# Optimization experiments

Measured on AMD Instinct MI355X. Metric: run time of the kernel, lower is better.

## Reference

```python
import jax, jax.numpy as jnp
import numpy as np

B, N, D, K, NUM_ITERS, EPS = 256, 4096, 64, 16, 3, 1e-8
LN_EPS = 1e-5


def ln(x, g, b):
    m = jnp.mean(x, axis=-1, keepdims=True)
    v = jnp.mean(jnp.square(x - m), axis=-1, keepdims=True)
    return (x - m) * jax.lax.rsqrt(v + LN_EPS) * g + b


def setup_inputs() -> dict:
    key = jax.random.key(0)
    ks = jax.random.split(key, 12)
    w = lambda k, s: jax.random.normal(k, s, dtype=jnp.float32) * 0.02
    return {
        "inputs": jax.random.normal(ks[0], (B, N, D), dtype=jnp.float32),
        "mask": jnp.ones((B, N), dtype=bool),
        "noise": jax.random.normal(ks[1], (B, K, D), dtype=jnp.float32),
        "slot_mu": w(ks[2], (1, 1, D)),
        "slot_logvar": jnp.zeros((1, 1, D), dtype=jnp.float32),
        "wq": w(ks[3], (D, D)), "bq": jnp.zeros((D,), jnp.float32),
        "wk": w(ks[4], (D, D)), "bk": jnp.zeros((D,), jnp.float32),
        "wv": w(ks[5], (D, D)), "bv": jnp.zeros((D,), jnp.float32),
        "w_ih": w(ks[6], (3 * D, D)), "w_hh": w(ks[7], (3 * D, D)),
        "b_ih": jnp.zeros((3 * D,), jnp.float32), "b_hh": jnp.zeros((3 * D,), jnp.float32),
        "g_in": jnp.ones((D,), jnp.float32), "b_in": jnp.zeros((D,), jnp.float32),
        "g_sl": jnp.ones((D,), jnp.float32), "b_sl": jnp.zeros((D,), jnp.float32),
        "g_mlp": jnp.ones((D,), jnp.float32), "b_mlp": jnp.zeros((D,), jnp.float32),
        "w1": w(ks[8], (2 * D, D)), "b1": jnp.zeros((2 * D,), jnp.float32),
        "w2": w(ks[9], (D, 2 * D)), "b2": jnp.zeros((D,), jnp.float32),
    }


def reference(inputs, mask, noise, slot_mu, slot_logvar, wq, bq, wk, bk, wv, bv,
              w_ih, w_hh, b_ih, b_hh, g_in, b_in, g_sl, b_sl, g_mlp, b_mlp,
              w1, b1, w2, b2):
    scale = D ** (-0.5)
    # init slots from learned Gaussian (noise passed explicitly for determinism)
    slots = slot_mu + jnp.exp(0.5 * slot_logvar) * noise  # (B,K,D)
    x = ln(inputs, g_in, b_in)
    k = x @ wk.T + bk  # (B,N,D)
    v = x @ wv.T + bv
    neg = jnp.where(mask, 0.0, -1e9).astype(x.dtype)[:, None, :]  # (B,1,N)

    def attend(s):
        q = ln(s, g_sl, b_sl) @ wq.T + bq
        logits = jnp.einsum('bkd,bnd->bkn', q, k) * scale + neg
        return jax.nn.softmax(logits, axis=1)  # competition over slots

    for _ in range(NUM_ITERS):
        slots_prev = slots
        attn = attend(slots)
        attn = attn + EPS
        attn = attn / jnp.sum(attn, axis=-1, keepdims=True)
        upd = jnp.einsum('bkn,bnd->bkd', attn, v)
        # torch GRUCell: gates order r, z, n
        gx = upd @ w_ih.T + b_ih          # (B,K,3D)
        gh = slots_prev @ w_hh.T + b_hh
        xr, xz, xn = jnp.split(gx, 3, axis=-1)
        hr, hz, hn = jnp.split(gh, 3, axis=-1)
        r = jax.nn.sigmoid(xr + hr)
        z = jax.nn.sigmoid(xz + hz)
        n = jnp.tanh(xn + r * hn)
        slots = (1.0 - z) * n + z * slots_prev
        h = ln(slots, g_mlp, b_mlp)
        slots = slots + jax.nn.relu(h @ w1.T + b1) @ w2.T + b2

    attn = attend(slots)
    return slots, attn
```

## Files before the change

kernel.cpp:

```cpp
#include <hip/hip_runtime.h>
#include <hip/hip_bf16.h>
#include <stdint.h>

#define B_ 256
#define N_ 4096
#define D_ 64
#define K_ 16
#define EPS_ 1e-8f
#define LN_EPS_ 1e-5f

typedef __attribute__((ext_vector_type(8))) short short8;
typedef __attribute__((ext_vector_type(4))) float f32x4;

__device__ __forceinline__ unsigned short f2bf(float f) {
  unsigned u = __builtin_bit_cast(unsigned, f);
  u += 0x7fffu + ((u >> 16) & 1u);
  return (unsigned short)(u >> 16);
}

__device__ __forceinline__ float sum4(f32x4 x) { return x[0] + x[1] + x[2] + x[3]; }

__device__ __forceinline__ float wsum64(float v) {
  v += __shfl_xor(v, 1); v += __shfl_xor(v, 2); v += __shfl_xor(v, 4);
  v += __shfl_xor(v, 8); v += __shfl_xor(v, 16); v += __shfl_xor(v, 32);
  return v;
}

template<int MODE, int LOADBF, int STORECACHE>
__global__ __launch_bounds__(256)
void attend2(const float* __restrict__ inputs,
             unsigned short* __restrict__ xcache,
             const float* __restrict__ g_in, const float* __restrict__ b_in,
             const float* __restrict__ q2w, const float* __restrict__ qcw,
             float* __restrict__ U, float* __restrict__ S,
             float* __restrict__ attn_out)
{
  const int b = blockIdx.y;
  const int chunk = blockIdx.x;
  const int wave = threadIdx.x >> 6;
  const int lane = threadIdx.x & 63;
  const int n = lane & 15;
  const int quad = lane >> 4;

  __shared__ unsigned short xbt[4][64][40];
  __shared__ unsigned short pbuf[4][16][40];
  __shared__ float redS[4][16];

  const float* qp = q2w + b * 1024 + n * 64 + quad * 8;
  short8 qa0, qa1;
#pragma unroll
  for (int j = 0; j < 8; ++j) {
    qa0[j] = (short)f2bf(qp[j]);
    qa1[j] = (short)f2bf(qp[32 + j]);
  }
  float qc[4];
#pragma unroll
  for (int r = 0; r < 4; ++r) qc[r] = qcw[b * 16 + quad * 4 + r];

  f32x4 gi[4], bi[4];
  if constexpr (!LOADBF) {
    gi[0] = *(const f32x4*)(g_in + quad * 8);       gi[1] = *(const f32x4*)(g_in + quad * 8 + 4);
    gi[2] = *(const f32x4*)(g_in + 32 + quad * 8);  gi[3] = *(const f32x4*)(g_in + 36 + quad * 8);
    bi[0] = *(const f32x4*)(b_in + quad * 8);       bi[1] = *(const f32x4*)(b_in + quad * 8 + 4);
    bi[2] = *(const f32x4*)(b_in + 32 + quad * 8);  bi[3] = *(const f32x4*)(b_in + 36 + quad * 8);
  }

  f32x4 Uacc[4];
#pragma unroll
  for (int t = 0; t < 4; ++t) Uacc[t] = (f32x4){0.f, 0.f, 0.f, 0.f};
  float Sacc[4] = {0.f, 0.f, 0.f, 0.f};

  const int rowwave = chunk * 1024 + wave * 256;

  for (int g = 0; g < 8; ++g) {
#pragma unroll
    for (int sub = 0; sub < 2; ++sub) {
      const int row = rowwave + g * 32 + sub * 16 + n;
      short8 xlo, xhi;
      if constexpr (LOADBF) {
        const unsigned short* xp = xcache + ((size_t)(b * N_ + row)) * 64 + quad * 8;
        xlo = __builtin_bit_cast(short8, *(const f32x4*)xp);
        xhi = __builtin_bit_cast(short8, *(const f32x4*)(xp + 32));
      } else {
        const float* bp = inputs + ((size_t)(b * N_ + row)) * 64;
        f32x4 a0 = *(const f32x4*)(bp + quad * 8);
        f32x4 a1 = *(const f32x4*)(bp + quad * 8 + 4);
        f32x4 a2 = *(const f32x4*)(bp + 32 + quad * 8);
        f32x4 a3 = *(const f32x4*)(bp + 36 + quad * 8);
        float s = sum4(a0) + sum4(a1) + sum4(a2) + sum4(a3);
        s += __shfl_xor(s, 16); s += __shfl_xor(s, 32);
        const float m = s * (1.f / 64.f);
        f32x4 d0 = a0 - m, d1 = a1 - m, d2 = a2 - m, d3 = a3 - m;
        float v = sum4(d0 * d0) + sum4(d1 * d1) + sum4(d2 * d2) + sum4(d3 * d3);
        v += __shfl_xor(v, 16); v += __shfl_xor(v, 32);
        const float rs = rsqrtf(v * (1.f / 64.f) + LN_EPS_);
        f32x4 y0 = d0 * rs * gi[0] + bi[0];
        f32x4 y1 = d1 * rs * gi[1] + bi[1];
        f32x4 y2 = d2 * rs * gi[2] + bi[2];
        f32x4 y3 = d3 * rs * gi[3] + bi[3];
#pragma unroll
        for (int j = 0; j < 4; ++j) {
          xlo[j]     = (short)f2bf(y0[j]);
          xlo[4 + j] = (short)f2bf(y1[j]);
          xhi[j]     = (short)f2bf(y2[j]);
          xhi[4 + j] = (short)f2bf(y3[j]);
        }
        if constexpr (STORECACHE) {
          unsigned short* sp = xcache + ((size_t)(b * N_ + row)) * 64 + quad * 8;
          *(f32x4*)sp = __builtin_bit_cast(f32x4, xlo);
          *(f32x4*)(sp + 32) = __builtin_bit_cast(f32x4, xhi);
        }
      }

      f32x4 c = __builtin_amdgcn_mfma_f32_16x16x32_bf16(qa0, xlo, (f32x4){0.f, 0.f, 0.f, 0.f}, 0, 0, 0);
      c = __builtin_amdgcn_mfma_f32_16x16x32_bf16(qa1, xhi, c, 0, 0, 0);

      float l[4];
#pragma unroll
      for (int r = 0; r < 4; ++r) l[r] = (c[r] + qc[r]) * 0.125f;
      float mx = fmaxf(fmaxf(l[0], l[1]), fmaxf(l[2], l[3]));
      mx = fmaxf(mx, __shfl_xor(mx, 16));
      mx = fmaxf(mx, __shfl_xor(mx, 32));
      float e[4], es = 0.f;
#pragma unroll
      for (int r = 0; r < 4; ++r) { e[r] = __expf(l[r] - mx); es += e[r]; }
      es += __shfl_xor(es, 16); es += __shfl_xor(es, 32);
      const float rinv = 1.f / es;

      if constexpr (MODE == 2) {
#pragma unroll
        for (int r = 0; r < 4; ++r)
          attn_out[((size_t)b * 16 + quad * 4 + r) * N_ + row] = e[r] * rinv;
      } else {
#pragma unroll
        for (int r = 0; r < 4; ++r) {
          const float p = e[r] * rinv;
          Sacc[r] += p;
          pbuf[wave][quad * 4 + r][sub * 16 + n] = f2bf(p);
        }
#pragma unroll
        for (int j = 0; j < 8; ++j) {
          xbt[wave][quad * 8 + j][sub * 16 + n]      = (unsigned short)xlo[j];
          xbt[wave][32 + quad * 8 + j][sub * 16 + n] = (unsigned short)xhi[j];
        }
      }
    }

    if constexpr (MODE != 2) {
      short8 pa = *(const short8*)&pbuf[wave][n][quad * 8];
#pragma unroll
      for (int t = 0; t < 4; ++t) {
        short8 bx = *(const short8*)&xbt[wave][t * 16 + n][quad * 8];
        Uacc[t] = __builtin_amdgcn_mfma_f32_16x16x32_bf16(pa, bx, Uacc[t], 0, 0, 0);
      }
    }
  }

  if constexpr (MODE == 2) return;

#pragma unroll
  for (int r = 0; r < 4; ++r) {
    float sv = Sacc[r];
    sv += __shfl_xor(sv, 1); sv += __shfl_xor(sv, 2);
    sv += __shfl_xor(sv, 4); sv += __shfl_xor(sv, 8);
    if (n == 0) redS[wave][quad * 4 + r] = sv;
  }
  __syncthreads();
  float* red = (float*)&xbt[0][0][0];
#pragma unroll
  for (int t = 0; t < 4; ++t)
#pragma unroll
    for (int r = 0; r < 4; ++r)
      red[(t * 4 + r) * 256 + wave * 64 + lane] = Uacc[t][r];
  __syncthreads();
#pragma unroll
  for (int ii = 0; ii < 4; ++ii) {
    const int i = wave * 4 + ii;
    const float sum = red[i * 256 + lane] + red[i * 256 + 64 + lane] +
                      red[i * 256 + 128 + lane] + red[i * 256 + 192 + lane];
    const int t = i >> 2, r = i & 3;
    atomicAdd(&U[b * 1024 + (quad * 4 + r) * 64 + t * 16 + n], sum);
  }
  if (threadIdx.x < 16) {
    const float ss = redS[0][threadIdx.x] + redS[1][threadIdx.x] +
                     redS[2][threadIdx.x] + redS[3][threadIdx.x];
    atomicAdd(&S[b * 16 + threadIdx.x], ss);
  }
}

__global__ __launch_bounds__(256)
void mid_kernel(int iter,
                const float* __restrict__ noise, const float* __restrict__ mu,
                const float* __restrict__ logvar,
                const float* __restrict__ wq, const float* __restrict__ bq,
                const float* __restrict__ wk, const float* __restrict__ bk,
                const float* __restrict__ wv, const float* __restrict__ bv,
                const float* __restrict__ w_ih, const float* __restrict__ w_hh,
                const float* __restrict__ b_ih, const float* __restrict__ b_hh,
                const float* __restrict__ g_sl, const float* __restrict__ b_sl,
                const float* __restrict__ g_mlp, const float* __restrict__ b_mlp,
                const float* __restrict__ w1, const float* __restrict__ b1,
                const float* __restrict__ w2, const float* __restrict__ b2,
                float* __restrict__ slots_ws, float* __restrict__ q2w, float* __restrict__ qcw,
                const float* __restrict__ U, const float* __restrict__ S,
                float* __restrict__ out_slots)
{
  const int b = blockIdx.x;
  const int tid = threadIdx.x;
  __shared__ float sl[1024];
  __shared__ float snew[1024];
  __shared__ float updx[1024];
  __shared__ float upds[1024];
  __shared__ float gx[3072];
  __shared__ float gh[3072];
  __shared__ float hh[1024];
  __shared__ float t1[2048];
  __shared__ float qv[1024];

  if (iter == 0) {
    for (int idx = tid; idx < 1024; idx += 256) {
      int d = idx & 63;
      snew[idx] = mu[d] + expf(0.5f * logvar[d]) * noise[(size_t)b * 1024 + idx];
    }
    __syncthreads();
  } else {
    for (int idx = tid; idx < 1024; idx += 256) sl[idx] = slots_ws[b * 1024 + idx];
    for (int idx = tid; idx < 1024; idx += 256) {
      int kk = idx >> 6;
      float denom = S[b * 16 + kk] + (float)N_ * EPS_;
      updx[idx] = U[b * 1024 + idx] / denom;
    }
    __syncthreads();
    for (int idx = tid; idx < 1024; idx += 256) {
      int kk = idx >> 6, d = idx & 63;
      float acc = bv[d];
      for (int e = 0; e < 64; ++e) acc += updx[kk * 64 + e] * wv[d * 64 + e];
      upds[idx] = acc;
    }
    __syncthreads();
    for (int idx = tid; idx < 3072; idx += 256) {
      int kk = idx / 192, j = idx % 192;
      float ax = b_ih[j], ah = b_hh[j];
      for (int d = 0; d < 64; ++d) {
        ax += upds[kk * 64 + d] * w_ih[j * 64 + d];
        ah += sl[kk * 64 + d] * w_hh[j * 64 + d];
      }
      gx[idx] = ax;
      gh[idx] = ah;
    }
    __syncthreads();
    for (int idx = tid; idx < 1024; idx += 256) {
      int kk = idx >> 6, d = idx & 63;
      float xr_ = gx[kk * 192 + d], xz_ = gx[kk * 192 + 64 + d], xn_ = gx[kk * 192 + 128 + d];
      float hr_ = gh[kk * 192 + d], hz_ = gh[kk * 192 + 64 + d], hn_ = gh[kk * 192 + 128 + d];
      float r_ = 1.f / (1.f + expf(-(xr_ + hr_)));
      float z_ = 1.f / (1.f + expf(-(xz_ + hz_)));
      float n_ = tanhf(xn_ + r_ * hn_);
      snew[idx] = (1.f - z_) * n_ + z_ * sl[idx];
    }
    __syncthreads();
    {
      int wv_ = tid >> 6, lane = tid & 63;
      for (int kk = wv_; kk < 16; kk += 4) {
        float v = snew[kk * 64 + lane];
        float m = wsum64(v) * (1.f / 64.f);
        float dd = v - m;
        float var = wsum64(dd * dd) * (1.f / 64.f);
        hh[kk * 64 + lane] = dd * rsqrtf(var + LN_EPS_) * g_mlp[lane] + b_mlp[lane];
      }
    }
    __syncthreads();
    for (int idx = tid; idx < 2048; idx += 256) {
      int kk = idx >> 7, j = idx & 127;
      float acc = b1[j];
      for (int d = 0; d < 64; ++d) acc += hh[kk * 64 + d] * w1[j * 64 + d];
      t1[idx] = fmaxf(acc, 0.f);
    }
    __syncthreads();
    for (int idx = tid; idx < 1024; idx += 256) {
      int kk = idx >> 6, d = idx & 63;
      float acc = b2[d];
      for (int j = 0; j < 128; ++j) acc += t1[kk * 128 + j] * w2[d * 128 + j];
      snew[idx] += acc;
    }
    __syncthreads();
  }

  for (int idx = tid; idx < 1024; idx += 256) {
    slots_ws[b * 1024 + idx] = snew[idx];
    if (iter == 3) out_slots[b * 1024 + idx] = snew[idx];
  }
  {
    int wv_ = tid >> 6, lane = tid & 63;
    for (int kk = wv_; kk < 16; kk += 4) {
      float v = snew[kk * 64 + lane];
      float m = wsum64(v) * (1.f / 64.f);
      float dd = v - m;
      float var = wsum64(dd * dd) * (1.f / 64.f);
      hh[kk * 64 + lane] = dd * rsqrtf(var + LN_EPS_) * g_sl[lane] + b_sl[lane];
    }
  }
  __syncthreads();
  for (int idx = tid; idx < 1024; idx += 256) {
    int kk = idx >> 6, d = idx & 63;
    float acc = bq[d];
    for (int e = 0; e < 64; ++e) acc += hh[kk * 64 + e] * wq[d * 64 + e];
    qv[idx] = acc;
  }
  __syncthreads();
  for (int idx = tid; idx < 1024; idx += 256) {
    int kk = idx >> 6, e = idx & 63;
    float acc = 0.f;
    for (int d = 0; d < 64; ++d) acc += qv[kk * 64 + d] * wk[d * 64 + e];
    q2w[b * 1024 + idx] = acc;
  }
  if (tid < 16) {
    float acc = 0.f;
    for (int d = 0; d < 64; ++d) acc += qv[tid * 64 + d] * bk[d];
    qcw[b * 16 + tid] = acc;
  }
}

extern "C" void kernel_launch(void* const* d_in, const int* in_sizes, int n_in,
                              void* d_out, int out_size, void* d_ws, size_t ws_size,
                              hipStream_t stream) {
  const float* inputs = (const float*)d_in[0];
  const float* noise  = (const float*)d_in[2];
  const float* mu     = (const float*)d_in[3];
  const float* logvar = (const float*)d_in[4];
  const float* wq   = (const float*)d_in[5];
  const float* bq   = (const float*)d_in[6];
  const float* wk   = (const float*)d_in[7];
  const float* bk   = (const float*)d_in[8];
  const float* wv   = (const float*)d_in[9];
  const float* bv   = (const float*)d_in[10];
  const float* w_ih = (const float*)d_in[11];
  const float* w_hh = (const float*)d_in[12];
  const float* b_ih = (const float*)d_in[13];
  const float* b_hh = (const float*)d_in[14];
  const float* g_in = (const float*)d_in[15];
  const float* b_in = (const float*)d_in[16];
  const float* g_sl = (const float*)d_in[17];
  const float* b_sl = (const float*)d_in[18];
  const float* g_mlp = (const float*)d_in[19];
  const float* b_mlp = (const float*)d_in[20];
  const float* w1 = (const float*)d_in[21];
  const float* b1 = (const float*)d_in[22];
  const float* w2 = (const float*)d_in[23];
  const float* b2 = (const float*)d_in[24];

  float* out_slots = (float*)d_out;
  float* attn_out = out_slots + B_ * K_ * D_;

  float* ws = (float*)d_ws;
  float* slots_ws = ws;
  float* q2w = ws + 262144;
  float* qcw = ws + 524288;
  float* U   = ws + 528384;
  float* S   = ws + 790528;
  unsigned short* xcache = (unsigned short*)(ws + 794624);
  const size_t need = (size_t)794624 * 4 + (size_t)B_ * N_ * D_ * 2;
  const bool cached = ws_size >= need;

  dim3 agrid(4, B_), ablock(256);

#define MID(it) mid_kernel<<<256, 256, 0, stream>>>(it, noise, mu, logvar, wq, bq, wk, bk, wv, bv, \
      w_ih, w_hh, b_ih, b_hh, g_sl, b_sl, g_mlp, b_mlp, w1, b1, w2, b2, \
      slots_ws, q2w, qcw, U, S, out_slots)
#define ATT(M, L, SC) attend2<M, L, SC><<<agrid, ablock, 0, stream>>>(inputs, xcache, g_in, b_in, \
      q2w, qcw, U, S, attn_out)

  MID(0);
  hipMemsetAsync(U, 0, (262144 + 4096) * sizeof(float), stream);
  if (cached) ATT(1, 0, 1); else ATT(1, 0, 0);
  MID(1);
  hipMemsetAsync(U, 0, (262144 + 4096) * sizeof(float), stream);
  if (cached) ATT(1, 1, 0); else ATT(1, 0, 0);
  MID(2);
  hipMemsetAsync(U, 0, (262144 + 4096) * sizeof(float), stream);
  if (cached) ATT(1, 1, 0); else ATT(1, 0, 0);
  MID(3);
  if (cached) ATT(2, 1, 0); else ATT(2, 0, 0);
#undef MID
#undef ATT
}
```

Measured before the change: 785.9 us.

## Prefetch next rows, drop softmax max, use exp2, and double attend grid chunks

```diff
diff --git a/kernel.cpp b/kernel.cpp
--- a/kernel.cpp
+++ b/kernel.cpp
@@ -8,6 +8,8 @@
 #define K_ 16
 #define EPS_ 1e-8f
 #define LN_EPS_ 1e-5f
+#define CHUNKS_ 8
+#define SUBS_ (N_ / CHUNKS_ / 4 / 16)
 
 typedef __attribute__((ext_vector_type(8))) short short8;
 typedef __attribute__((ext_vector_type(4))) float f32x4;
@@ -27,7 +29,7 @@
 }
 
 template<int MODE, int LOADBF, int STORECACHE>
-__global__ __launch_bounds__(256)
+__global__ __launch_bounds__(256, (LOADBF ? 5 : 4))
 void attend2(const float* __restrict__ inputs,
              unsigned short* __restrict__ xcache,
              const float* __restrict__ g_in, const float* __restrict__ b_in,
@@ -53,9 +55,10 @@
     qa0[j] = (short)f2bf(qp[j]);
     qa1[j] = (short)f2bf(qp[32 + j]);
   }
-  float qc[4];
-#pragma unroll
-  for (int r = 0; r < 4; ++r) qc[r] = qcw[b * 16 + quad * 4 + r];
+  const float SC = 0.125f * 1.44269504088896f;
+  float qc2[4];
+#pragma unroll
+  for (int r = 0; r < 4; ++r) qc2[r] = qcw[b * 16 + quad * 4 + r] * SC;
 
   f32x4 gi[4], bi[4];
   if constexpr (!LOADBF) {
@@ -70,90 +73,102 @@
   for (int t = 0; t < 4; ++t) Uacc[t] = (f32x4){0.f, 0.f, 0.f, 0.f};
   float Sacc[4] = {0.f, 0.f, 0.f, 0.f};
 
-  const int rowwave = chunk * 1024 + wave * 256;
-
-  for (int g = 0; g < 8; ++g) {
-#pragma unroll
-    for (int sub = 0; sub < 2; ++sub) {
-      const int row = rowwave + g * 32 + sub * 16 + n;
-      short8 xlo, xhi;
-      if constexpr (LOADBF) {
-        const unsigned short* xp = xcache + ((size_t)(b * N_ + row)) * 64 + quad * 8;
-        xlo = __builtin_bit_cast(short8, *(const f32x4*)xp);
-        xhi = __builtin_bit_cast(short8, *(const f32x4*)(xp + 32));
-      } else {
-        const float* bp = inputs + ((size_t)(b * N_ + row)) * 64;
-        f32x4 a0 = *(const f32x4*)(bp + quad * 8);
-        f32x4 a1 = *(const f32x4*)(bp + quad * 8 + 4);
-        f32x4 a2 = *(const f32x4*)(bp + 32 + quad * 8);
-        f32x4 a3 = *(const f32x4*)(bp + 36 + quad * 8);
-        float s = sum4(a0) + sum4(a1) + sum4(a2) + sum4(a3);
-        s += __shfl_xor(s, 16); s += __shfl_xor(s, 32);
-        const float m = s * (1.f / 64.f);
-        f32x4 d0 = a0 - m, d1 = a1 - m, d2 = a2 - m, d3 = a3 - m;
-        float v = sum4(d0 * d0) + sum4(d1 * d1) + sum4(d2 * d2) + sum4(d3 * d3);
-        v += __shfl_xor(v, 16); v += __shfl_xor(v, 32);
-        const float rs = rsqrtf(v * (1.f / 64.f) + LN_EPS_);
-        f32x4 y0 = d0 * rs * gi[0] + bi[0];
-        f32x4 y1 = d1 * rs * gi[1] + bi[1];
-        f32x4 y2 = d2 * rs * gi[2] + bi[2];
-        f32x4 y3 = d3 * rs * gi[3] + bi[3];
-#pragma unroll
-        for (int j = 0; j < 4; ++j) {
-          xlo[j]     = (short)f2bf(y0[j]);
-          xlo[4 + j] = (short)f2bf(y1[j]);
-          xhi[j]     = (short)f2bf(y2[j]);
-          xhi[4 + j] = (short)f2bf(y3[j]);
+  const int rowwave = chunk * (N_ / CHUNKS_) + wave * (N_ / CHUNKS_ / 4);
+
+  auto LOADRAW = [&](int s, f32x4& A0, f32x4& A1, f32x4& A2, f32x4& A3) {
+    const int row = rowwave + s * 16 + n;
+    if constexpr (LOADBF) {
+      const unsigned short* xp = xcache + ((size_t)(b * N_ + row)) * 64 + quad * 8;
+      A0 = *(const f32x4*)xp;
+      A1 = *(const f32x4*)(xp + 32);
+    } else {
+      const float* bp = inputs + ((size_t)(b * N_ + row)) * 64;
+      A0 = *(const f32x4*)(bp + quad * 8);
+      A1 = *(const f32x4*)(bp + quad * 8 + 4);
+      A2 = *(const f32x4*)(bp + 32 + quad * 8);
+      A3 = *(const f32x4*)(bp + 36 + quad * 8);
+    }
+  };
+
+  f32x4 ca0, ca1, ca2, ca3;
+  LOADRAW(0, ca0, ca1, ca2, ca3);
+
+#pragma unroll
+  for (int s = 0; s < SUBS_; ++s) {
+    f32x4 na0, na1, na2, na3;
+    LOADRAW((s + 1) & (SUBS_ - 1), na0, na1, na2, na3);
+
+    const int row = rowwave + s * 16 + n;
+    const int sub = s & 1;
+
+    short8 xlo, xhi;
+    if constexpr (LOADBF) {
+      xlo = __builtin_bit_cast(short8, ca0);
+      xhi = __builtin_bit_cast(short8, ca1);
+    } else {
+      f32x4 a0 = ca0, a1 = ca1, a2 = ca2, a3 = ca3;
+      float sm = sum4(a0) + sum4(a1) + sum4(a2) + sum4(a3);
+      sm += __shfl_xor(sm, 16); sm += __shfl_xor(sm, 32);
+      const float m = sm * (1.f / 64.f);
+      f32x4 d0 = a0 - m, d1 = a1 - m, d2 = a2 - m, d3 = a3 - m;
+      float v = sum4(d0 * d0) + sum4(d1 * d1) + sum4(d2 * d2) + sum4(d3 * d3);
+      v += __shfl_xor(v, 16); v += __shfl_xor(v, 32);
+      const float rs = rsqrtf(v * (1.f / 64.f) + LN_EPS_);
+      f32x4 y0 = d0 * rs * gi[0] + bi[0];
+      f32x4 y1 = d1 * rs * gi[1] + bi[1];
+      f32x4 y2 = d2 * rs * gi[2] + bi[2];
+      f32x4 y3 = d3 * rs * gi[3] + bi[3];
+#pragma unroll
+      for (int j = 0; j < 4; ++j) {
+        xlo[j]     = (short)f2bf(y0[j]);
+        xlo[4 + j] = (short)f2bf(y1[j]);
+        xhi[j]     = (short)f2bf(y2[j]);
+        xhi[4 + j] = (short)f2bf(y3[j]);
+      }
+      if constexpr (STORECACHE) {
+        unsigned short* sp = xcache + ((size_t)(b * N_ + row)) * 64 + quad * 8;
+        *(f32x4*)sp = __builtin_bit_cast(f32x4, xlo);
+        *(f32x4*)(sp + 32) = __builtin_bit_cast(f32x4, xhi);
+      }
+    }
+
+    f32x4 c = __builtin_amdgcn_mfma_f32_16x16x32_bf16(qa0, xlo, (f32x4){0.f, 0.f, 0.f, 0.f}, 0, 0, 0);
+    c = __builtin_amdgcn_mfma_f32_16x16x32_bf16(qa1, xhi, c, 0, 0, 0);
+
+    float e[4], es = 0.f;
+#pragma unroll
+    for (int r = 0; r < 4; ++r) { e[r] = exp2f(c[r] * SC + qc2[r]); es += e[r]; }
+    es += __shfl_xor(es, 16); es += __shfl_xor(es, 32);
+    const float rinv = __builtin_amdgcn_rcpf(es);
+
+    if constexpr (MODE == 2) {
+#pragma unroll
+      for (int r = 0; r < 4; ++r)
+        attn_out[((size_t)b * 16 + quad * 4 + r) * N_ + row] = e[r] * rinv;
+    } else {
+#pragma unroll
+      for (int r = 0; r < 4; ++r) {
+        const float p = e[r] * rinv;
+        Sacc[r] += p;
+        pbuf[wave][quad * 4 + r][sub * 16 + n] = f2bf(p);
+      }
+#pragma unroll
+      for (int j = 0; j < 8; ++j) {
+        xbt[wave][quad * 8 + j][sub * 16 + n]      = (unsigned short)xlo[j];
+        xbt[wave][32 + quad * 8 + j][sub * 16 + n] = (unsigned short)xhi[j];
+      }
+
+      if (sub == 1) {
+        short8 pa = *(const short8*)&pbuf[wave][n][quad * 8];
+#pragma unroll
+        for (int t = 0; t < 4; ++t) {
+          short8 bx = *(const short8*)&xbt[wave][t * 16 + n][quad * 8];
+          Uacc[t] = __builtin_amdgcn_mfma_f32_16x16x32_bf16(pa, bx, Uacc[t], 0, 0, 0);
         }
-        if constexpr (STORECACHE) {
-          unsigned short* sp = xcache + ((size_t)(b * N_ + row)) * 64 + quad * 8;
-          *(f32x4*)sp = __builtin_bit_cast(f32x4, xlo);
-          *(f32x4*)(sp + 32) = __builtin_bit_cast(f32x4, xhi);
-        }
-      }
-
-      f32x4 c = __builtin_amdgcn_mfma_f32_16x16x32_bf16(qa0, xlo, (f32x4){0.f, 0.f, 0.f, 0.f}, 0, 0, 0);
-      c = __builtin_amdgcn_mfma_f32_16x16x32_bf16(qa1, xhi, c, 0, 0, 0);
-
-      float l[4];
-#pragma unroll
-      for (int r = 0; r < 4; ++r) l[r] = (c[r] + qc[r]) * 0.125f;
-      float mx = fmaxf(fmaxf(l[0], l[1]), fmaxf(l[2], l[3]));
-      mx = fmaxf(mx, __shfl_xor(mx, 16));
-      mx = fmaxf(mx, __shfl_xor(mx, 32));
-      float e[4], es = 0.f;
-#pragma unroll
-      for (int r = 0; r < 4; ++r) { e[r] = __expf(l[r] - mx); es += e[r]; }
-      es += __shfl_xor(es, 16); es += __shfl_xor(es, 32);
-      const float rinv = 1.f / es;
-
-      if constexpr (MODE == 2) {
-#pragma unroll
-        for (int r = 0; r < 4; ++r)
-          attn_out[((size_t)b * 16 + quad * 4 + r) * N_ + row] = e[r] * rinv;
-      } else {
-#pragma unroll
-        for (int r = 0; r < 4; ++r) {
-          const float p = e[r] * rinv;
-          Sacc[r] += p;
-          pbuf[wave][quad * 4 + r][sub * 16 + n] = f2bf(p);
-        }
-#pragma unroll
-        for (int j = 0; j < 8; ++j) {
-          xbt[wave][quad * 8 + j][sub * 16 + n]      = (unsigned short)xlo[j];
-          xbt[wave][32 + quad * 8 + j][sub * 16 + n] = (unsigned short)xhi[j];
-        }
-      }
-    }
-
-    if constexpr (MODE != 2) {
-      short8 pa = *(const short8*)&pbuf[wave][n][quad * 8];
-#pragma unroll
-      for (int t = 0; t < 4; ++t) {
-        short8 bx = *(const short8*)&xbt[wave][t * 16 + n][quad * 8];
-        Uacc[t] = __builtin_amdgcn_mfma_f32_16x16x32_bf16(pa, bx, Uacc[t], 0, 0, 0);
-      }
-    }
+      }
+    }
+
+    ca0 = na0; ca1 = na1; ca2 = na2; ca3 = na3;
   }
 
   if constexpr (MODE == 2) return;
@@ -362,7 +377,7 @@
   const size_t need = (size_t)794624 * 4 + (size_t)B_ * N_ * D_ * 2;
   const bool cached = ws_size >= need;
 
-  dim3 agrid(4, B_), ablock(256);
+  dim3 agrid(CHUNKS_, B_), ablock(256);
 
 #define MID(it) mid_kernel<<<256, 256, 0, stream>>>(it, noise, mu, logvar, wq, bq, wk, bk, wv, bv, \
       w_ih, w_hh, b_ih, b_hh, g_sl, b_sl, g_mlp, b_mlp, w1, b1, w2, b2, \
```

After: 853.1 us. 1.09x slower.
